# Performance work log

Hardware: AMD Instinct MI355X
Metric: run time of the kernel (lower is better)

The kernel has to match this reference:

```python
import jax, jax.numpy as jnp
import numpy as np

H = W = 252
C_IN = 384
NB_ANCHORS = 4
NB_CLASSES = 4


def setup_inputs() -> dict:
    key = jax.random.key(0)
    ks = jax.random.split(key, 13)
    s = 1.0 / np.sqrt(C_IN)
    def w(k, o):
        return jax.random.uniform(k, (o, C_IN), jnp.float32, -s, s)
    def b(k, o):
        return jax.random.uniform(k, (o,), jnp.float32, -s, s)
    return {
        "x": jax.random.normal(ks[0], (4, H, W, C_IN), jnp.float32),
        "occ_w": w(ks[1], NB_ANCHORS),      "occ_b": b(ks[2], NB_ANCHORS),
        "loc_w": w(ks[3], 3 * NB_ANCHORS),  "loc_b": b(ks[4], 3 * NB_ANCHORS),
        "angle_w": w(ks[5], NB_ANCHORS),    "angle_b": b(ks[6], NB_ANCHORS),
        "size_w": w(ks[7], 3 * NB_ANCHORS), "size_b": b(ks[8], 3 * NB_ANCHORS),
        "head_w": w(ks[9], NB_ANCHORS),     "head_b": b(ks[10], NB_ANCHORS),
        "clf_w": w(ks[11], NB_ANCHORS * NB_CLASSES), "clf_b": b(ks[12], NB_ANCHORS * NB_CLASSES),
    }


def _proj(x, w, b):
    # 1x1 conv in NHWC == per-pixel GEMM: [B,H,W,Cin] x [O,Cin] -> [B,H,W,O]
    return jnp.einsum("bhwc,oc->bhwo", x, w) + b


def reference(x, occ_w, occ_b, loc_w, loc_b, angle_w, angle_b,
              size_w, size_b, head_w, head_b, clf_w, clf_b):
    B = x.shape[0]
    occ = jax.nn.sigmoid(_proj(x, occ_w, occ_b))                       # [B,H,W,4]
    loc = _proj(x, loc_w, loc_b).reshape(B, H, W, NB_ANCHORS, 3)       # [B,H,W,4,3]
    angle = _proj(x, angle_w, angle_b)                                 # [B,H,W,4]
    size = _proj(x, size_w, size_b).reshape(B, H, W, NB_ANCHORS, 3)    # [B,H,W,4,3]
    heading = jax.nn.sigmoid(_proj(x, head_w, head_b))                 # [B,H,W,4]
    clf = _proj(x, clf_w, clf_b).reshape(B, H, W, NB_ANCHORS, NB_CLASSES)  # [B,H,W,4,4]
    return (occ, loc, angle, size, heading, clf)
```

## Files before the change

### kernel.cpp

```cpp
#include <hip/hip_runtime.h>


#define HH 252
#define WW 252
#define BB 4
#define CIN 384
#define PIX (BB*HH*WW)
#define NPAD 64
#define KPAD 392
#define WIMG_USHORTS (NPAD*KPAD)
#define WIMG_BYTES (WIMG_USHORTS*2)
#define LDS_BYTES (WIMG_BYTES + NPAD*4)

typedef __attribute__((ext_vector_type(8))) short short8;
typedef __attribute__((ext_vector_type(4))) float f32x4;
typedef __attribute__((ext_vector_type(4))) unsigned int uint4v;

__device__ __forceinline__ unsigned bfpk(float a, float b) {
  unsigned ua = __float_as_uint(a), ub = __float_as_uint(b);
  ua = (ua + 0x7FFFu + ((ua >> 16) & 1u)) >> 16;
  ub = (ub + 0x7FFFu + ((ub >> 16) & 1u)) >> 16;
  return ua | (ub << 16);
}
__device__ __forceinline__ unsigned short f2bf(float a) {
  unsigned ua = __float_as_uint(a);
  return (unsigned short)((ua + 0x7FFFu + ((ua >> 16) & 1u)) >> 16);
}

__global__ void prep_kernel(
    const float* __restrict__ occ_w, const float* __restrict__ occ_b,
    const float* __restrict__ loc_w, const float* __restrict__ loc_b,
    const float* __restrict__ ang_w, const float* __restrict__ ang_b,
    const float* __restrict__ siz_w, const float* __restrict__ siz_b,
    const float* __restrict__ hea_w, const float* __restrict__ hea_b,
    const float* __restrict__ clf_w, const float* __restrict__ clf_b,
    unsigned short* __restrict__ wimg, float* __restrict__ bimg) {
  int idx = blockIdx.x * 256 + threadIdx.x;
  if (idx < WIMG_USHORTS) {
    int n = idx / KPAD, k = idx % KPAD;
    float v = 0.f;
    if (k < CIN) {
      const float* w = nullptr; int lo = 0;
      if      (n < 4)  { w = occ_w; lo = n; }
      else if (n < 16) { w = loc_w; lo = n - 4; }
      else if (n < 20) { w = ang_w; lo = n - 16; }
      else if (n < 32) { w = siz_w; lo = n - 20; }
      else if (n < 36) { w = hea_w; lo = n - 32; }
      else if (n < 52) { w = clf_w; lo = n - 36; }
      if (w) v = w[lo * CIN + k];
    }
    wimg[idx] = f2bf(v);
  } else if (idx < WIMG_USHORTS + NPAD) {
    int c = idx - WIMG_USHORTS;
    float v = 0.f;
    if      (c < 4)  v = occ_b[c];
    else if (c < 16) v = loc_b[c - 4];
    else if (c < 20) v = ang_b[c - 16];
    else if (c < 32) v = siz_b[c - 20];
    else if (c < 36) v = hea_b[c - 32];
    else if (c < 52) v = clf_b[c - 36];
    bimg[c] = v;
  }
}

__global__ __launch_bounds__(256, 3) void head_kernel(
    const float* __restrict__ x, const uint4v* __restrict__ wsimg,
    float* __restrict__ out) {
  __shared__ __align__(16) unsigned char lds_raw[LDS_BYTES];
  {
    uint4v* dst = (uint4v*)lds_raw;
    for (int u = threadIdx.x; u < LDS_BYTES / 16; u += 256) dst[u] = wsimg[u];
  }
  __syncthreads();
  const unsigned short* Wl = (const unsigned short*)lds_raw;
  const float* biasl = (const float*)(lds_raw + WIMG_BYTES);

  const int lane = threadIdx.x & 63;
  const int wave = threadIdx.x >> 6;
  const int m = lane & 15;
  const int quad = lane >> 4;
  const int pixel_base = blockIdx.x * 64 + wave * 16;
  const float* xrow = x + (size_t)(pixel_base + m) * CIN + quad * 8;

  f32x4 acc0 = {0.f, 0.f, 0.f, 0.f};
  f32x4 acc1 = {0.f, 0.f, 0.f, 0.f};
  f32x4 acc2 = {0.f, 0.f, 0.f, 0.f};
  f32x4 acc3 = {0.f, 0.f, 0.f, 0.f};

  const unsigned short* wbase = Wl + (size_t)m * KPAD + quad * 8;

  #pragma unroll 4
  for (int kit = 0; kit < 12; ++kit) {
    const f32x4* px = (const f32x4*)(xrow + kit * 32);
    f32x4 f0 = px[0];
    f32x4 f1 = px[1];
    union { unsigned u[4]; short8 s; } a;
    a.u[0] = bfpk(f0.x, f0.y);
    a.u[1] = bfpk(f0.z, f0.w);
    a.u[2] = bfpk(f1.x, f1.y);
    a.u[3] = bfpk(f1.z, f1.w);
    const unsigned short* wk = wbase + kit * 32;
    short8 b0 = *(const short8*)(wk);
    short8 b1 = *(const short8*)(wk + 16 * KPAD);
    short8 b2 = *(const short8*)(wk + 32 * KPAD);
    short8 b3 = *(const short8*)(wk + 48 * KPAD);
    acc0 = __builtin_amdgcn_mfma_f32_16x16x32_bf16(a.s, b0, acc0, 0, 0, 0);
    acc1 = __builtin_amdgcn_mfma_f32_16x16x32_bf16(a.s, b1, acc1, 0, 0, 0);
    acc2 = __builtin_amdgcn_mfma_f32_16x16x32_bf16(a.s, b2, acc2, 0, 0, 0);
    acc3 = __builtin_amdgcn_mfma_f32_16x16x32_bf16(a.s, b3, acc3, 0, 0, 0);
  }

  f32x4 accs[4] = {acc0, acc1, acc2, acc3};
  #pragma unroll
  for (int nt = 0; nt < 4; ++nt) {
    int c = nt * 16 + m;
    if (c < 52) {
      size_t base; int stride, ch; bool sig = false;
      if      (c < 4)  { base = 0;                stride = 4;  ch = c;      sig = true; }
      else if (c < 16) { base = (size_t)PIX * 4;  stride = 12; ch = c - 4;  }
      else if (c < 20) { base = (size_t)PIX * 16; stride = 4;  ch = c - 16; }
      else if (c < 32) { base = (size_t)PIX * 20; stride = 12; ch = c - 20; }
      else if (c < 36) { base = (size_t)PIX * 32; stride = 4;  ch = c - 32; sig = true; }
      else             { base = (size_t)PIX * 36; stride = 16; ch = c - 36; }
      float bv = biasl[c];
      #pragma unroll
      for (int r = 0; r < 4; ++r) {
        int p = pixel_base + quad * 4 + r;
        float v = accs[nt][r] + bv;
        if (sig) v = 1.f / (1.f + __expf(-v));
        out[base + (size_t)p * stride + ch] = v;
      }
    }
  }
}

extern "C" void kernel_launch(void* const* d_in, const int* in_sizes, int n_in,
                              void* d_out, int out_size, void* d_ws, size_t ws_size,
                              hipStream_t stream) {
  const float* x     = (const float*)d_in[0];
  const float* occ_w = (const float*)d_in[1];
  const float* occ_b = (const float*)d_in[2];
  const float* loc_w = (const float*)d_in[3];
  const float* loc_b = (const float*)d_in[4];
  const float* ang_w = (const float*)d_in[5];
  const float* ang_b = (const float*)d_in[6];
  const float* siz_w = (const float*)d_in[7];
  const float* siz_b = (const float*)d_in[8];
  const float* hea_w = (const float*)d_in[9];
  const float* hea_b = (const float*)d_in[10];
  const float* clf_w = (const float*)d_in[11];
  const float* clf_b = (const float*)d_in[12];

  unsigned short* wimg = (unsigned short*)d_ws;
  float* bimg = (float*)((char*)d_ws + WIMG_BYTES);

  prep_kernel<<<(WIMG_USHORTS + NPAD + 255) / 256, 256, 0, stream>>>(
      occ_w, occ_b, loc_w, loc_b, ang_w, ang_b, siz_w, siz_b, hea_w, hea_b,
      clf_w, clf_b, wimg, bimg);

  head_kernel<<<PIX / 64, 256, 0, stream>>>(x, (const uint4v*)d_ws,
                                            (float*)d_out);
}
```

Baseline: 546.7 us.

## Fuse weight prep into head kernel and process three pixel tiles per block

Removes the separate prep kernel launch: each block converts the fp32 weights to bf16 and writes the padded image straight into LDS. Each block now handles three 64-pixel tiles, so the LDS weight staging cost is spread over three times as many pixels and the B fragments are reused across tiles. The trade-off is redundant weight conversion in every block and more accumulator registers per thread, which could reduce occupancy.

```diff
diff --git a/kernel.cpp b/kernel.cpp
--- a/kernel.cpp
+++ b/kernel.cpp
@@ -11,10 +11,12 @@
 #define WIMG_USHORTS (NPAD*KPAD)
 #define WIMG_BYTES (WIMG_USHORTS*2)
 #define LDS_BYTES (WIMG_BYTES + NPAD*4)
+#define TILES_PB 3
+#define PIX_PB (TILES_PB*64)
+#define NBLOCKS (PIX / PIX_PB)
 
 typedef __attribute__((ext_vector_type(8))) short short8;
 typedef __attribute__((ext_vector_type(4))) float f32x4;
-typedef __attribute__((ext_vector_type(4))) unsigned int uint4v;
 
 __device__ __forceinline__ unsigned bfpk(float a, float b) {
   unsigned ua = __float_as_uint(a), ub = __float_as_uint(b);
@@ -22,113 +24,120 @@
   ub = (ub + 0x7FFFu + ((ub >> 16) & 1u)) >> 16;
   return ua | (ub << 16);
 }
-__device__ __forceinline__ unsigned short f2bf(float a) {
-  unsigned ua = __float_as_uint(a);
-  return (unsigned short)((ua + 0x7FFFu + ((ua >> 16) & 1u)) >> 16);
-}
 
-__global__ void prep_kernel(
+__global__ __launch_bounds__(256, 3) void head_kernel(
+    const float* __restrict__ x,
     const float* __restrict__ occ_w, const float* __restrict__ occ_b,
     const float* __restrict__ loc_w, const float* __restrict__ loc_b,
     const float* __restrict__ ang_w, const float* __restrict__ ang_b,
     const float* __restrict__ siz_w, const float* __restrict__ siz_b,
     const float* __restrict__ hea_w, const float* __restrict__ hea_b,
     const float* __restrict__ clf_w, const float* __restrict__ clf_b,
-    unsigned short* __restrict__ wimg, float* __restrict__ bimg) {
-  int idx = blockIdx.x * 256 + threadIdx.x;
-  if (idx < WIMG_USHORTS) {
-    int n = idx / KPAD, k = idx % KPAD;
-    float v = 0.f;
-    if (k < CIN) {
-      const float* w = nullptr; int lo = 0;
+    float* __restrict__ out) {
+  __shared__ __align__(16) unsigned char lds_raw[LDS_BYTES];
+  unsigned short* Wl = (unsigned short*)lds_raw;
+  float* biasl = (float*)(lds_raw + WIMG_BYTES);
+
+  for (int c = threadIdx.x; c < NPAD * 49; c += 256) {
+    int n = c / 49, k8 = c - n * 49;
+    short8 v = {0, 0, 0, 0, 0, 0, 0, 0};
+    if (k8 < 48 && n < 52) {
+      const float* w; int lo;
       if      (n < 4)  { w = occ_w; lo = n; }
       else if (n < 16) { w = loc_w; lo = n - 4; }
       else if (n < 20) { w = ang_w; lo = n - 16; }
       else if (n < 32) { w = siz_w; lo = n - 20; }
       else if (n < 36) { w = hea_w; lo = n - 32; }
-      else if (n < 52) { w = clf_w; lo = n - 36; }
-      if (w) v = w[lo * CIN + k];
+      else             { w = clf_w; lo = n - 36; }
+      const f32x4* src = (const f32x4*)(w + lo * CIN + k8 * 8);
+      f32x4 f0 = src[0], f1 = src[1];
+      union { unsigned u[4]; short8 s; } t;
+      t.u[0] = bfpk(f0.x, f0.y);
+      t.u[1] = bfpk(f0.z, f0.w);
+      t.u[2] = bfpk(f1.x, f1.y);
+      t.u[3] = bfpk(f1.z, f1.w);
+      v = t.s;
     }
-    wimg[idx] = f2bf(v);
-  } else if (idx < WIMG_USHORTS + NPAD) {
-    int c = idx - WIMG_USHORTS;
-    float v = 0.f;
-    if      (c < 4)  v = occ_b[c];
-    else if (c < 16) v = loc_b[c - 4];
-    else if (c < 20) v = ang_b[c - 16];
-    else if (c < 32) v = siz_b[c - 20];
-    else if (c < 36) v = hea_b[c - 32];
-    else if (c < 52) v = clf_b[c - 36];
-    bimg[c] = v;
+    *(short8*)(Wl + (size_t)n * KPAD + k8 * 8) = v;
   }
-}
-
-__global__ __launch_bounds__(256, 3) void head_kernel(
-    const float* __restrict__ x, const uint4v* __restrict__ wsimg,
-    float* __restrict__ out) {
-  __shared__ __align__(16) unsigned char lds_raw[LDS_BYTES];
-  {
-    uint4v* dst = (uint4v*)lds_raw;
-    for (int u = threadIdx.x; u < LDS_BYTES / 16; u += 256) dst[u] = wsimg[u];
+  if (threadIdx.x < NPAD) {
+    int c = threadIdx.x;
+    float bv = 0.f;
+    if      (c < 4)  bv = occ_b[c];
+    else if (c < 16) bv = loc_b[c - 4];
+    else if (c < 20) bv = ang_b[c - 16];
+    else if (c < 32) bv = siz_b[c - 20];
+    else if (c < 36) bv = hea_b[c - 32];
+    else if (c < 52) bv = clf_b[c - 36];
+    biasl[c] = bv;
   }
   __syncthreads();
-  const unsigned short* Wl = (const unsigned short*)lds_raw;
-  const float* biasl = (const float*)(lds_raw + WIMG_BYTES);
 
   const int lane = threadIdx.x & 63;
   const int wave = threadIdx.x >> 6;
   const int m = lane & 15;
   const int quad = lane >> 4;
-  const int pixel_base = blockIdx.x * 64 + wave * 16;
-  const float* xrow = x + (size_t)(pixel_base + m) * CIN + quad * 8;
-
-  f32x4 acc0 = {0.f, 0.f, 0.f, 0.f};
-  f32x4 acc1 = {0.f, 0.f, 0.f, 0.f};
-  f32x4 acc2 = {0.f, 0.f, 0.f, 0.f};
-  f32x4 acc3 = {0.f, 0.f, 0.f, 0.f};
-
   const unsigned short* wbase = Wl + (size_t)m * KPAD + quad * 8;
 
-  #pragma unroll 4
+  int pbase[TILES_PB];
+  const float* xrow[TILES_PB];
+  #pragma unroll
+  for (int t = 0; t < TILES_PB; ++t) {
+    pbase[t] = blockIdx.x * PIX_PB + t * 64 + wave * 16;
+    xrow[t] = x + (size_t)(pbase[t] + m) * CIN + quad * 8;
+  }
+
+  f32x4 acc[TILES_PB][4];
+  #pragma unroll
+  for (int t = 0; t < TILES_PB; ++t)
+    #pragma unroll
+    for (int n = 0; n < 4; ++n) acc[t][n] = (f32x4){0.f, 0.f, 0.f, 0.f};
+
+  #pragma unroll 2
   for (int kit = 0; kit < 12; ++kit) {
-    const f32x4* px = (const f32x4*)(xrow + kit * 32);
-    f32x4 f0 = px[0];
-    f32x4 f1 = px[1];
-    union { unsigned u[4]; short8 s; } a;
-    a.u[0] = bfpk(f0.x, f0.y);
-    a.u[1] = bfpk(f0.z, f0.w);
-    a.u[2] = bfpk(f1.x, f1.y);
-    a.u[3] = bfpk(f1.z, f1.w);
     const unsigned short* wk = wbase + kit * 32;
     short8 b0 = *(const short8*)(wk);
     short8 b1 = *(const short8*)(wk + 16 * KPAD);
     short8 b2 = *(const short8*)(wk + 32 * KPAD);
     short8 b3 = *(const short8*)(wk + 48 * KPAD);
-    acc0 = __builtin_amdgcn_mfma_f32_16x16x32_bf16(a.s, b0, acc0, 0, 0, 0);
-    acc1 = __builtin_amdgcn_mfma_f32_16x16x32_bf16(a.s, b1, acc1, 0, 0, 0);
-    acc2 = __builtin_amdgcn_mfma_f32_16x16x32_bf16(a.s, b2, acc2, 0, 0, 0);
-    acc3 = __builtin_amdgcn_mfma_f32_16x16x32_bf16(a.s, b3, acc3, 0, 0, 0);
+    #pragma unroll
+    for (int t = 0; t < TILES_PB; ++t) {
+      const f32x4* px = (const f32x4*)(xrow[t] + kit * 32);
+      f32x4 f0 = px[0];
+      f32x4 f1 = px[1];
+      union { unsigned u[4]; short8 s; } a;
+      a.u[0] = bfpk(f0.x, f0.y);
+      a.u[1] = bfpk(f0.z, f0.w);
+      a.u[2] = bfpk(f1.x, f1.y);
+      a.u[3] = bfpk(f1.z, f1.w);
+      acc[t][0] = __builtin_amdgcn_mfma_f32_16x16x32_bf16(a.s, b0, acc[t][0], 0, 0, 0);
+      acc[t][1] = __builtin_amdgcn_mfma_f32_16x16x32_bf16(a.s, b1, acc[t][1], 0, 0, 0);
+      acc[t][2] = __builtin_amdgcn_mfma_f32_16x16x32_bf16(a.s, b2, acc[t][2], 0, 0, 0);
+      acc[t][3] = __builtin_amdgcn_mfma_f32_16x16x32_bf16(a.s, b3, acc[t][3], 0, 0, 0);
+    }
   }
 
-  f32x4 accs[4] = {acc0, acc1, acc2, acc3};
   #pragma unroll
-  for (int nt = 0; nt < 4; ++nt) {
-    int c = nt * 16 + m;
-    if (c < 52) {
-      size_t base; int stride, ch; bool sig = false;
-      if      (c < 4)  { base = 0;                stride = 4;  ch = c;      sig = true; }
-      else if (c < 16) { base = (size_t)PIX * 4;  stride = 12; ch = c - 4;  }
-      else if (c < 20) { base = (size_t)PIX * 16; stride = 4;  ch = c - 16; }
-      else if (c < 32) { base = (size_t)PIX * 20; stride = 12; ch = c - 20; }
-      else if (c < 36) { base = (size_t)PIX * 32; stride = 4;  ch = c - 32; sig = true; }
-      else             { base = (size_t)PIX * 36; stride = 16; ch = c - 36; }
-      float bv = biasl[c];
-      #pragma unroll
-      for (int r = 0; r < 4; ++r) {
-        int p = pixel_base + quad * 4 + r;
-        float v = accs[nt][r] + bv;
-        if (sig) v = 1.f / (1.f + __expf(-v));
-        out[base + (size_t)p * stride + ch] = v;
+  for (int t = 0; t < TILES_PB; ++t) {
+    #pragma unroll
+    for (int nt = 0; nt < 4; ++nt) {
+      int c = nt * 16 + m;
+      if (c < 52) {
+        size_t base; int stride, ch; bool sig = false;
+        if      (c < 4)  { base = 0;                stride = 4;  ch = c;      sig = true; }
+        else if (c < 16) { base = (size_t)PIX * 4;  stride = 12; ch = c - 4;  }
+        else if (c < 20) { base = (size_t)PIX * 16; stride = 4;  ch = c - 16; }
+        else if (c < 32) { base = (size_t)PIX * 20; stride = 12; ch = c - 20; }
+        else if (c < 36) { base = (size_t)PIX * 32; stride = 4;  ch = c - 32; sig = true; }
+        else             { base = (size_t)PIX * 36; stride = 16; ch = c - 36; }
+        float bv = biasl[c];
+        #pragma unroll
+        for (int r = 0; r < 4; ++r) {
+          int p = pbase[t] + quad * 4 + r;
+          float v = acc[t][nt][r] + bv;
+          if (sig) v = 1.f / (1.f + __expf(-v));
+          out[base + (size_t)p * stride + ch] = v;
+        }
       }
     }
   }
@@ -151,13 +160,7 @@
   const float* clf_w = (const float*)d_in[11];
   const float* clf_b = (const float*)d_in[12];
 
-  unsigned short* wimg = (unsigned short*)d_ws;
-  float* bimg = (float*)((char*)d_ws + WIMG_BYTES);
-
-  prep_kernel<<<(WIMG_USHORTS + NPAD + 255) / 256, 256, 0, stream>>>(
-      occ_w, occ_b, loc_w, loc_b, ang_w, ang_b, siz_w, siz_b, hea_w, hea_b,
-      clf_w, clf_b, wimg, bimg);
-
-  head_kernel<<<PIX / 64, 256, 0, stream>>>(x, (const uint4v*)d_ws,
-                                            (float*)d_out);
+  head_kernel<<<NBLOCKS, 256, 0, stream>>>(
+      x, occ_w, occ_b, loc_w, loc_b, ang_w, ang_b, siz_w, siz_b,
+      hea_w, hea_b, clf_w, clf_b, (float*)d_out);
 }
```

New measurement: 559.6 us. 1.02x slower.
